# Performance work log

Hardware: AMD Instinct MI355X
Metric: run time of the kernel (lower is better)

Reference implementation:

```python
import jax, jax.numpy as jnp
import numpy as np

NUM_HEADS = 16
KEY_DIM = 64
D_MODEL = 1024
SUPPORTS = 128


def _gaussian_orthogonal_random_matrix(m, d, seed=0):
    # GOR sampler with scaling=0: orthogonal blocks, rows rescaled by norms of iid Gaussian rows.
    rng = np.random.RandomState(seed)
    blocks = []
    n_full = m // d
    for _ in range(n_full):
        q, _ = np.linalg.qr(rng.randn(d, d))
        blocks.append(q.T)
    rem = m - n_full * d
    if rem > 0:
        q, _ = np.linalg.qr(rng.randn(d, d))
        blocks.append(q.T[:rem])
    W = np.concatenate(blocks, axis=0)  # [m, d], orthonormal rows per block
    multiplier = np.linalg.norm(rng.randn(m, d), axis=1)  # chi(d) row norms
    return (multiplier[:, None] * W).astype(np.float32)


def setup_inputs() -> dict:
    key0 = jax.random.key(0)
    ks = jax.random.split(key0, 12)
    B, S, D, H, K = 4, 4096, D_MODEL, NUM_HEADS, KEY_DIM
    glorot_in = lambda k, shape, fan_in, fan_out: jax.random.uniform(
        k, shape, jnp.float32, -1.0, 1.0) * np.sqrt(6.0 / (fan_in + fan_out))
    return {
        "query": jax.random.normal(ks[0], (B, S, D), jnp.float32),
        "value": jax.random.normal(ks[1], (B, S, D), jnp.float32),
        "key": jax.random.normal(ks[2], (B, S, D), jnp.float32),
        "Wq": glorot_in(ks[3], (D, H, K), D, H * K),
        "bq": jnp.zeros((H, K), jnp.float32),
        "Wk": glorot_in(ks[4], (D, H, K), D, H * K),
        "bk": jnp.zeros((H, K), jnp.float32),
        "Wv": glorot_in(ks[5], (D, H, K), D, H * K),
        "bv": jnp.zeros((H, K), jnp.float32),
        "Wo": glorot_in(ks[6], (H, K, D), H * K, D),
        "bo": jnp.zeros((D,), jnp.float32),
        "proj": jnp.asarray(_gaussian_orthogonal_random_matrix(SUPPORTS, K)),
    }


def kernel_feature_creator(data, projection, is_query):
    # FAVOR+ positive softmax-kernel features: phi(x) = exp(w.x' - |x'|^2/2 - stab)/sqrt(m)
    d = data.shape[-1]
    m = projection.shape[0]
    x = data * (d ** -0.25)  # so that q'.k' = q.k / sqrt(d)
    wx = jnp.einsum("bshk,mk->bshm", x, projection)
    diag = 0.5 * jnp.sum(x * x, axis=-1, keepdims=True)
    if is_query:
        stab = jax.lax.stop_gradient(jnp.max(wx, axis=-1, keepdims=True))
    else:
        stab = jax.lax.stop_gradient(jnp.max(wx))
    return jnp.exp(wx - diag - stab) * (m ** -0.5)


def reference(query, value, key, Wq, bq, Wk, bk, Wv, bv, Wo, bo, proj):
    # EinsumDense projections: [B,S,D] -> [B,S,H,K]
    q = jnp.einsum("bsd,dhk->bshk", query, Wq) + bq
    k = jnp.einsum("bsd,dhk->bshk", key, Wk) + bk
    v = jnp.einsum("bsd,dhk->bshk", value, Wv) + bv
    phi_q = kernel_feature_creator(q, proj, True)   # [B,T,H,M]
    phi_k = kernel_feature_creator(k, proj, False)  # [B,S,H,M]
    kv = jnp.einsum("bshm,bshd->bhmd", phi_k, v)
    qkv = jnp.einsum("bthm,bhmd->bthd", phi_q, kv)
    # normalisation: D = phi_q . (sum_s phi_k)
    k1 = jnp.sum(phi_k, axis=1)                     # [B,H,M]
    denom = jnp.einsum("bthm,bhm->bth", phi_q, k1)
    out = qkv * (1.0 / (denom + 1e-6))[..., None]
    return jnp.einsum("bthd,hdo->bto", out, Wo) + bo
```

## Files before the change

### kernel.cpp

```cpp
#include <hip/hip_runtime.h>
#include <hip/hip_bf16.h>


#define B_  4
#define S_  4096
#define H_  16

#define SCALE_X 0.3535533905932738f
#define CM      0.08838834764831845f

typedef __attribute__((ext_vector_type(8))) short bf16x8;
typedef __attribute__((ext_vector_type(4))) short s16x4;
typedef __attribute__((ext_vector_type(8))) unsigned short u16x8;
typedef __attribute__((ext_vector_type(8))) _Float16 f16x8;
typedef __attribute__((ext_vector_type(4))) _Float16 f16x4;
typedef __attribute__((ext_vector_type(4))) float f32x4;

#define OFF_A    ((size_t)0)
#define OFF_B    ((size_t)16777216)
#define OFF_X    ((size_t)33554432)
#define OFF_KV   ((size_t)37814272)
#define OFF_K1   ((size_t)38338560)
#define OFF_BM   ((size_t)38346752)
#define OFF_ST   ((size_t)38347264)
#define OFF_A16  ((size_t)38347776)

__device__ __forceinline__ unsigned short f2bf(float x) {
  union { __hip_bfloat16 b; unsigned short u; } c;
  c.b = __float2bfloat16(x);
  return c.u;
}

#define MFMAB(ACC, A, B)                                               \
  ACC = __builtin_amdgcn_mfma_f32_16x16x32_bf16(A, B, ACC, 0, 0, 0)

#define GLDS(GP, LP)                                                  \
  __builtin_amdgcn_global_load_lds(                                   \
      (const __attribute__((address_space(1))) unsigned int*)(GP),    \
      (__attribute__((address_space(3))) unsigned int*)(LP), 16, 0, 0)

__device__ __forceinline__ void load_pfrag(const float* __restrict__ proj, int m,
                                           int kb, bf16x8* ph) {
  const float* p = proj + m * 64 + kb;
  float4 a = *reinterpret_cast<const float4*>(p);
  float4 b = *reinterpret_cast<const float4*>(p + 4);
  float v[8] = {a.x, a.y, a.z, a.w, b.x, b.y, b.z, b.w};
  bf16x8 h;
#pragma unroll
  for (int j = 0; j < 8; ++j) h[j] = (short)f2bf(v[j]);
  *ph = h;
}

#define STAGE_XR(XV, WANT_DIAG)                                           \
  {                                                                       \
    f16x8 xv_ = (XV);                                                     \
    u16x8 hh_;                                                            \
    float sq_ = 0.f;                                                      \
    _Pragma("unroll") for (int j = 0; j < 8; ++j) {                       \
      float vf_ = (float)xv_[j] * SCALE_X;                                \
      sq_ += vf_ * vf_;                                                   \
      hh_[j] = f2bf(vf_);                                                 \
    }                                                                     \
    *reinterpret_cast<u16x8*>(&Xh[srow][xc]) = hh_;                       \
    if (WANT_DIAG) {                                                      \
      sq_ += __shfl_xor(sq_, 1);                                          \
      sq_ += __shfl_xor(sq_, 2);                                          \
      sq_ += __shfl_xor(sq_, 4);                                          \
      if ((tid & 7) == 0) diags[srow] = 0.5f * sq_;                       \
    }                                                                     \
  }

#define WX_COMPUTE(WX)                                                       \
  _Pragma("unroll") for (int st_ = 0; st_ < 2; ++st_)                        \
  _Pragma("unroll") for (int ks_ = 0; ks_ < 2; ++ks_) {                      \
    const int rr_ = st_ * 16 + l15;                                          \
    const int cc_ = ((ks_ * 4 + lg) ^ (l15 & 7)) << 3;                       \
    bf16x8 xh_ = *reinterpret_cast<const bf16x8*>(&Xh[rr_][cc_]);            \
    _Pragma("unroll") for (int mtl_ = 0; mtl_ < 2; ++mtl_)                   \
        MFMAB(WX[st_][mtl_], xh_, ph[mtl_][ks_]);                            \
  }

__global__ __launch_bounds__(256) void cvt_f16_kernel(
    const float* __restrict__ in, _Float16* __restrict__ out) {
  const size_t stride = (size_t)gridDim.x * 256 * 8;
  for (size_t i = ((size_t)blockIdx.x * 256 + threadIdx.x) * 8; i < 16777216UL;
       i += stride) {
    float4 a = *reinterpret_cast<const float4*>(in + i);
    float4 b = *reinterpret_cast<const float4*>(in + i + 4);
    f16x8 h;
    h[0] = (_Float16)a.x; h[1] = (_Float16)a.y;
    h[2] = (_Float16)a.z; h[3] = (_Float16)a.w;
    h[4] = (_Float16)b.x; h[5] = (_Float16)b.y;
    h[6] = (_Float16)b.z; h[7] = (_Float16)b.w;
    *reinterpret_cast<f16x8*>(out + i) = h;
  }
}

__global__ __launch_bounds__(256) void wt_f16_kernel(
    const float* __restrict__ W, _Float16* __restrict__ T) {
  __shared__ float t[32][33];
  const int tx = threadIdx.x & 31, ty = threadIdx.x >> 5;
  const int k0 = blockIdx.x * 32, n0 = blockIdx.y * 32;
#pragma unroll
  for (int i = 0; i < 4; ++i)
    t[ty + 8 * i][tx] = W[(size_t)(k0 + ty + 8 * i) * 1024 + n0 + tx];
  __syncthreads();
#pragma unroll
  for (int i = 0; i < 4; ++i)
    T[(size_t)(n0 + ty + 8 * i) * 1024 + k0 + tx] = (_Float16)t[tx][ty + 8 * i];
}

template <int F16OUT>
__global__ __launch_bounds__(512) void gemm_lds(
    const _Float16* __restrict__ A16, const _Float16* __restrict__ BT,
    const float* __restrict__ bias, void* __restrict__ Cout) {
  __shared__ _Float16 As[4][256][32];
  __shared__ _Float16 Bs[4][256][32];
  const int tid = threadIdx.x;
  const int bid = blockIdx.x;
  const int m0 = (bid & 63) << 8;
  const int n0 = (bid >> 6) << 8;
  const int wave = tid >> 6, lane = tid & 63;
  const int wm = (wave >> 2) << 7;
  const int wn = (wave & 3) << 6;
  const int l15 = lane & 15, lg = lane >> 4;

  const int rlo = tid >> 2;
  const int cg = ((tid & 3) ^ ((rlo >> 1) & 3)) << 3;
  const int wqbase = wave << 10;

  const _Float16* pa = A16 + (size_t)(m0 + rlo) * 1024 + cg;
  const _Float16* pb = BT + (size_t)(n0 + rlo) * 1024 + cg;

  f32x4 acc[8][4];
#pragma unroll
  for (int i = 0; i < 8; ++i)
#pragma unroll
    for (int j = 0; j < 4; ++j) acc[i][j] = f32x4{0.f, 0.f, 0.f, 0.f};

#define STAGE_T(nb, kt)                                                   \
  {                                                                       \
    char* la = (char*)&As[nb][0][0] + wqbase;                             \
    char* lb = (char*)&Bs[nb][0][0] + wqbase;                             \
    GLDS(pa + (kt) * 32, la);                                             \
    GLDS(pa + (kt) * 32 + 131072, la + 8192);                             \
    GLDS(pb + (kt) * 32, lb);                                             \
    GLDS(pb + (kt) * 32 + 131072, lb + 8192);                             \
  }

#define PIPE_BAR(N)                                                       \
  asm volatile("s_waitcnt vmcnt(" #N ")" ::: "memory");                   \
  __builtin_amdgcn_s_barrier();                                           \
  asm volatile("" ::: "memory");                                          \
  __builtin_amdgcn_sched_barrier(0);

#define COMPUTE(cur)                                                      \
  {                                                                       \
    f16x8 bf[4];                                                          \
    _Pragma("unroll") for (int fn = 0; fn < 4; ++fn) {                    \
      const int r = wn + fn * 16 + l15;                                   \
      bf[fn] = *reinterpret_cast<const f16x8*>(                           \
          &Bs[cur][r][(lg ^ ((r >> 1) & 3)) << 3]);                       \
    }                                                                     \
    _Pragma("unroll") for (int fm = 0; fm < 8; ++fm) {                    \
      const int r = wm + fm * 16 + l15;                                   \
      f16x8 av = *reinterpret_cast<const f16x8*>(                         \
          &As[cur][r][(lg ^ ((r >> 1) & 3)) << 3]);                       \
      _Pragma("unroll") for (int fn = 0; fn < 4; ++fn)                    \
        acc[fm][fn] = __builtin_amdgcn_mfma_f32_16x16x32_f16(             \
            av, bf[fn], acc[fm][fn], 0, 0, 0);                            \
    }                                                                     \
  }

  STAGE_T(0, 0);
  STAGE_T(1, 1);

  for (int kt = 0; kt < 30; ++kt) {
    STAGE_T((kt + 2) & 3, kt + 2);
    PIPE_BAR(8);
    COMPUTE(kt & 3);
  }
  PIPE_BAR(4);
  COMPUTE(2);
  PIPE_BAR(0);
  COMPUTE(3);

#pragma unroll
  for (int fm = 0; fm < 8; ++fm) {
    const int row = m0 + wm + fm * 16 + (lg << 2);
#pragma unroll
    for (int fn = 0; fn < 4; ++fn) {
      const int col = n0 + wn + fn * 16 + l15;
      const float bc = bias[col];
      f32x4 v = acc[fm][fn];
      if (F16OUT) {
        _Float16* C = (_Float16*)Cout;
#pragma unroll
        for (int j = 0; j < 4; ++j)
          C[(size_t)(row + j) * 1024 + col] = (_Float16)(v[j] + bc);
      } else {
        float* C = (float*)Cout;
#pragma unroll
        for (int j = 0; j < 4; ++j) C[(size_t)(row + j) * 1024 + col] = v[j] + bc;
      }
    }
  }
#undef STAGE_T
#undef PIPE_BAR
#undef COMPUTE
}

__global__ __launch_bounds__(256) void wxmax_mfma_kernel(
    const _Float16* __restrict__ kproj, const float* __restrict__ proj,
    float* __restrict__ blockmax) {
  __shared__ unsigned short Xh[32][64];
  __shared__ float diags[32];
  __shared__ float redw[4];
  const int tid = threadIdx.x, blk = blockIdx.x;
  const int lane = tid & 63, w = tid >> 6;
  const int l15 = lane & 15, lg = lane >> 4;
  (void)diags;

  bf16x8 ph[2][2];
#pragma unroll
  for (int mtl = 0; mtl < 2; ++mtl)
#pragma unroll
    for (int ks = 0; ks < 2; ++ks)
      load_pfrag(proj, (2 * w + mtl) * 16 + l15, ks * 32 + lg * 8, &ph[mtl][ks]);

  float gmax = -3.4e38f;
  const int srow = tid >> 3, q8 = (tid & 7) << 3;
  const int xc = ((q8 >> 3) ^ (srow & 7)) << 3;

  f16x8 xk = *reinterpret_cast<const f16x8*>(
      kproj + (size_t)(blk * 512 + srow) * 64 + q8);

  for (int batch = 0; batch < 16; ++batch) {
    STAGE_XR(xk, false);
    f16x8 xk2;
    if (batch < 15)
      xk2 = *reinterpret_cast<const f16x8*>(
          kproj + (size_t)(blk * 512 + (batch + 1) * 32 + srow) * 64 + q8);
    __syncthreads();
    f32x4 wx[2][2];
#pragma unroll
    for (int st = 0; st < 2; ++st)
#pragma unroll
      for (int mtl = 0; mtl < 2; ++mtl) wx[st][mtl] = f32x4{0, 0, 0, 0};
    WX_COMPUTE(wx);
#pragma unroll
    for (int st = 0; st < 2; ++st)
#pragma unroll
      for (int mtl = 0; mtl < 2; ++mtl)
#pragma unroll
        for (int r = 0; r < 4; ++r) gmax = fmaxf(gmax, wx[st][mtl][r]);
    __syncthreads();
    if (batch < 15) xk = xk2;
  }
#pragma unroll
  for (int off = 32; off; off >>= 1) gmax = fmaxf(gmax, __shfl_xor(gmax, off));
  if (lane == 0) redw[w] = gmax;
  __syncthreads();
  if (tid == 0)
    blockmax[blk] = fmaxf(fmaxf(redw[0], redw[1]), fmaxf(redw[2], redw[3]));
}

__global__ __launch_bounds__(256) void maxreduce_kernel(
    const float* __restrict__ blockmax, float* __restrict__ stab, int n) {
  __shared__ float sm[256];
  float v = -3.4e38f;
  for (int i = threadIdx.x; i < n; i += 256) v = fmaxf(v, blockmax[i]);
  sm[threadIdx.x] = v;
  __syncthreads();
  for (int s = 128; s; s >>= 1) {
    if (threadIdx.x < s)
      sm[threadIdx.x] = fmaxf(sm[threadIdx.x], sm[threadIdx.x + s]);
    __syncthreads();
  }
  if (threadIdx.x == 0) *stab = sm[0];
}

__global__ __launch_bounds__(256) void kv_mfma_kernel(
    const _Float16* __restrict__ kproj, const _Float16* __restrict__ vproj,
    const float* __restrict__ proj, const float* __restrict__ stabp,
    float* __restrict__ kvpartT, float* __restrict__ k1part) {
  __shared__ unsigned short Xh[32][64];
  __shared__ float Vs[32][66];
  __shared__ unsigned short phiTh[128][40];
  __shared__ float diags[32];
  const int tid = threadIdx.x, blk = blockIdx.x;
  const int c = blk & 15, bh = blk >> 4, b = bh >> 4, h = bh & 15;
  const int lane = tid & 63, w = tid >> 6;
  const int l15 = lane & 15, lg = lane >> 4;
  const float stab = *stabp;

  bf16x8 ph[2][2];
#pragma unroll
  for (int mtl = 0; mtl < 2; ++mtl)
#pragma unroll
    for (int ks = 0; ks < 2; ++ks)
      load_pfrag(proj, (2 * w + mtl) * 16 + l15, ks * 32 + lg * 8, &ph[mtl][ks]);

  f32x4 akv[2][4];
#pragma unroll
  for (int i = 0; i < 2; ++i)
#pragma unroll
    for (int j = 0; j < 4; ++j) akv[i][j] = f32x4{0, 0, 0, 0};
  float k1acc[2] = {0.f, 0.f};

  const int srow = tid >> 3, q8 = (tid & 7) << 3;
  const int xc = ((q8 >> 3) ^ (srow & 7)) << 3;

  size_t rb = (((size_t)(b * S_ + c * 256 + srow) * H_ + h)) << 6;
  f16x8 xk = *reinterpret_cast<const f16x8*>(kproj + rb + q8);
  f16x8 xv = *reinterpret_cast<const f16x8*>(vproj + rb + q8);

  for (int batch = 0; batch < 8; ++batch) {
    STAGE_XR(xk, true);
    {
#pragma unroll
      for (int j = 0; j < 8; ++j) Vs[srow][q8 + j] = (float)xv[j];
    }
    f16x8 xk2, xv2;
    if (batch < 7) {
      const size_t rb2 =
          (((size_t)(b * S_ + c * 256 + (batch + 1) * 32 + srow) * H_ + h)) << 6;
      xk2 = *reinterpret_cast<const f16x8*>(kproj + rb2 + q8);
      xv2 = *reinterpret_cast<const f16x8*>(vproj + rb2 + q8);
    }
    __syncthreads();

    f32x4 wx[2][2];
#pragma unroll
    for (int st = 0; st < 2; ++st)
#pragma unroll
      for (int mtl = 0; mtl < 2; ++mtl) wx[st][mtl] = f32x4{0, 0, 0, 0};
    WX_COMPUTE(wx);

#pragma unroll
    for (int st = 0; st < 2; ++st)
#pragma unroll
      for (int mtl = 0; mtl < 2; ++mtl) {
        const int m = (2 * w + mtl) * 16 + l15;
        s16x4 hv;
        float psum = 0.f;
#pragma unroll
        for (int r = 0; r < 4; ++r) {
          const int s = st * 16 + lg * 4 + r;
          float p = __expf(wx[st][mtl][r] - diags[s] - stab) * CM;
          psum += p;
          hv[r] = (short)f2bf(p);
        }
        k1acc[mtl] += psum;
        *reinterpret_cast<s16x4*>(&phiTh[m][st * 16 + lg * 4]) = hv;
      }
    __syncthreads();

    bf16x8 pah[2];
#pragma unroll
    for (int mtl = 0; mtl < 2; ++mtl)
      pah[mtl] = *reinterpret_cast<const bf16x8*>(
          &phiTh[(2 * w + mtl) * 16 + l15][lg * 8]);
#pragma unroll
    for (int dt = 0; dt < 4; ++dt) {
      bf16x8 bvh;
#pragma unroll
      for (int j = 0; j < 8; ++j)
        bvh[j] = (short)f2bf(Vs[lg * 8 + j][dt * 16 + l15]);
#pragma unroll
      for (int mtl = 0; mtl < 2; ++mtl) MFMAB(akv[mtl][dt], pah[mtl], bvh);
    }
    __syncthreads();
    if (batch < 7) {
      xk = xk2;
      xv = xv2;
    }
  }

#pragma unroll
  for (int mtl = 0; mtl < 2; ++mtl) {
#pragma unroll
    for (int dt = 0; dt < 4; ++dt) {
      const int d = dt * 16 + l15, m0 = (2 * w + mtl) * 16 + lg * 4;
      *reinterpret_cast<f32x4*>(&kvpartT[(size_t)blk * 8192 + d * 128 + m0]) =
          akv[mtl][dt];
    }
    float kk = k1acc[mtl];
    kk += __shfl_xor(kk, 16);
    kk += __shfl_xor(kk, 32);
    if (lane < 16) k1part[blk * 128 + (2 * w + mtl) * 16 + lane] = kk;
  }
}

__global__ __launch_bounds__(256) void kvreduce_kernel(
    const float* __restrict__ kvpartT, const float* __restrict__ k1part,
    unsigned short* __restrict__ kvT, float* __restrict__ k1) {
  const int bh = blockIdx.x;
  for (int i = threadIdx.x; i < 8192; i += 256) {
    float s = 0.f;
#pragma unroll
    for (int c = 0; c < 16; ++c) s += kvpartT[(size_t)(bh * 16 + c) * 8192 + i];
    kvT[(size_t)bh * 8192 + i] = f2bf(s);
  }
  if (threadIdx.x < 128) {
    float s = 0.f;
#pragma unroll
    for (int c = 0; c < 16; ++c) s += k1part[(bh * 16 + c) * 128 + threadIdx.x];
    k1[bh * 128 + threadIdx.x] = s;
  }
}

__global__ __launch_bounds__(256) void qkv_wave_kernel(
    const _Float16* __restrict__ qproj, const unsigned short* __restrict__ kvT,
    const float* __restrict__ k1g, const float* __restrict__ proj,
    _Float16* __restrict__ outh) {
  __shared__ unsigned short Pl[128][64];
  __shared__ unsigned short Kl[64][128];
  __shared__ unsigned short Phw[4][16][128];
  __shared__ float k1s[128];
  __shared__ float dgw[4][16];
  __shared__ float dnw[4][16];
  const int tid = threadIdx.x, blk = blockIdx.x;
  const int ch = blk & 31, bh = blk >> 5, b = bh >> 4, h = bh & 15;
  const int lane = tid & 63, w = tid >> 6;
  const int l15 = lane & 15, lg = lane >> 4;

  {
    const int r = tid >> 1;
    const int cb = (tid & 1) << 2;
#pragma unroll
    for (int j = 0; j < 4; ++j) {
      const int ck = cb + j;
      float4 a = *reinterpret_cast<const float4*>(proj + r * 64 + ck * 8);
      float4 bq = *reinterpret_cast<const float4*>(proj + r * 64 + ck * 8 + 4);
      float v[8] = {a.x, a.y, a.z, a.w, bq.x, bq.y, bq.z, bq.w};
      u16x8 hh;
#pragma unroll
      for (int q = 0; q < 8; ++q) hh[q] = f2bf(v[q]);
      *reinterpret_cast<u16x8*>(&Pl[r][(ck ^ (r & 7)) << 3]) = hh;
    }
    const int d = tid >> 2;
    const int kb = (tid & 3) << 2;
#pragma unroll
    for (int j = 0; j < 4; ++j) {
      const int ck = kb + j;
      u16x8 kk = *reinterpret_cast<const u16x8*>(
          kvT + (size_t)bh * 8192 + d * 128 + ck * 8);
      *reinterpret_cast<u16x8*>(&Kl[d][(ck ^ (d & 7)) << 3]) = kk;
    }
    if (tid < 128) k1s[tid] = k1g[bh * 128 + tid];
  }
  __syncthreads();

  float k1v[8];
#pragma unroll
  for (int mt = 0; mt < 8; ++mt) k1v[mt] = k1s[mt * 16 + l15];

#pragma unroll
  for (int it = 0; it < 2; ++it) {
    const int t0 = ch * 128 + w * 32 + it * 16;
    const size_t xrow = (((size_t)(b * S_ + t0 + l15) * H_ + h)) << 6;
    f16x8 x0 = *reinterpret_cast<const f16x8*>(qproj + xrow + lg * 8);
    f16x8 x1 = *reinterpret_cast<const f16x8*>(qproj + xrow + 32 + lg * 8);
    bf16x8 xb0, xb1;
    float sq = 0.f;
#pragma unroll
    for (int j = 0; j < 8; ++j) {
      float v0 = (float)x0[j] * SCALE_X;
      float v1 = (float)x1[j] * SCALE_X;
      sq += v0 * v0 + v1 * v1;
      xb0[j] = (short)f2bf(v0);
      xb1[j] = (short)f2bf(v1);
    }
    sq += __shfl_xor(sq, 16);
    sq += __shfl_xor(sq, 32);
    if (lg == 0) dgw[w][l15] = 0.5f * sq;

    f32x4 wxa[8];
#pragma unroll
    for (int mt = 0; mt < 8; ++mt) {
      wxa[mt] = f32x4{0.f, 0.f, 0.f, 0.f};
      bf16x8 p0 = *reinterpret_cast<const bf16x8*>(
          &Pl[mt * 16 + l15][((lg) ^ (l15 & 7)) << 3]);
      bf16x8 p1 = *reinterpret_cast<const bf16x8*>(
          &Pl[mt * 16 + l15][((4 + lg) ^ (l15 & 7)) << 3]);
      MFMAB(wxa[mt], xb0, p0);
      MFMAB(wxa[mt], xb1, p1);
    }

    float rmx[4];
#pragma unroll
    for (int r = 0; r < 4; ++r) {
      float v = wxa[0][r];
#pragma unroll
      for (int mt = 1; mt < 8; ++mt) v = fmaxf(v, wxa[mt][r]);
      v = fmaxf(v, __shfl_xor(v, 1));
      v = fmaxf(v, __shfl_xor(v, 2));
      v = fmaxf(v, __shfl_xor(v, 4));
      v = fmaxf(v, __shfl_xor(v, 8));
      rmx[r] = v;
    }
    float den[4] = {0.f, 0.f, 0.f, 0.f};
#pragma unroll
    for (int r = 0; r < 4; ++r) {
      const int trow = lg * 4 + r;
      const float off = rmx[r] + dgw[w][trow];
#pragma unroll
      for (int mt = 0; mt < 8; ++mt) {
        const int m = mt * 16 + l15;
        float p = __expf(wxa[mt][r] - off) * CM;
        den[r] += p * k1v[mt];
        Phw[w][trow][((((m >> 3)) ^ (trow & 7)) << 3) | (m & 7)] = f2bf(p);
      }
    }
#pragma unroll
    for (int r = 0; r < 4; ++r) {
      float v = den[r];
      v += __shfl_xor(v, 1);
      v += __shfl_xor(v, 2);
      v += __shfl_xor(v, 4);
      v += __shfl_xor(v, 8);
      if (l15 == 0) dnw[w][lg * 4 + r] = v;
    }

    const float dens = 1.f / (dnw[w][l15] + 1e-6f);
#pragma unroll
    for (int dt = 0; dt < 4; ++dt) {
      f32x4 od = {0.f, 0.f, 0.f, 0.f};
#pragma unroll
      for (int ks = 0; ks < 4; ++ks) {
        bf16x8 ka = *reinterpret_cast<const bf16x8*>(
            &Kl[dt * 16 + l15][((ks * 4 + lg) ^ (l15 & 7)) << 3]);
        bf16x8 bp = *reinterpret_cast<const bf16x8*>(
            &Phw[w][l15][((ks * 4 + lg) ^ (l15 & 7)) << 3]);
        MFMAB(od, ka, bp);
      }
      f16x4 o;
#pragma unroll
      for (int j = 0; j < 4; ++j) o[j] = (_Float16)(od[j] * dens);
      *reinterpret_cast<f16x4*>(
          &outh[(size_t)(b * S_ + t0 + l15) * 1024 + h * 64 + dt * 16 +
                lg * 4]) = o;
    }
  }
}

extern "C" void kernel_launch(void* const* d_in, const int* in_sizes, int n_in,
                              void* d_out, int out_size, void* d_ws,
                              size_t ws_size, hipStream_t stream) {
  const float* query = (const float*)d_in[0];
  const float* value = (const float*)d_in[1];
  const float* key   = (const float*)d_in[2];
  const float* Wq = (const float*)d_in[3];
  const float* bq = (const float*)d_in[4];
  const float* Wk = (const float*)d_in[5];
  const float* bk = (const float*)d_in[6];
  const float* Wv = (const float*)d_in[7];
  const float* bv = (const float*)d_in[8];
  const float* Wo = (const float*)d_in[9];
  const float* bo = (const float*)d_in[10];
  const float* proj = (const float*)d_in[11];
  float* out = (float*)d_out;
  float* ws = (float*)d_ws;

  _Float16* KP16 = (_Float16*)(ws + OFF_A);
  _Float16* VP16 = (_Float16*)(ws + OFF_B);
  _Float16* WT = (_Float16*)(ws + OFF_X);
  float* K1P = ws + OFF_X;
  unsigned short* KVT = (unsigned short*)(ws + OFF_KV);
  float* K1 = ws + OFF_K1;
  float* BMX = ws + OFF_BM;
  float* ST = ws + OFF_ST;
  _Float16* X16 = (_Float16*)(ws + OFF_A16);
  float* KVPT = ws + OFF_A16;

  dim3 gw(32, 32);

  cvt_f16_kernel<<<2048, 256, 0, stream>>>(key, X16);
  wt_f16_kernel<<<gw, 256, 0, stream>>>(Wk, WT);
  gemm_lds<1><<<256, 512, 0, stream>>>(X16, WT, bk, KP16);
  wxmax_mfma_kernel<<<512, 256, 0, stream>>>(KP16, proj, BMX);
  maxreduce_kernel<<<1, 256, 0, stream>>>(BMX, ST, 512);
  cvt_f16_kernel<<<2048, 256, 0, stream>>>(value, X16);
  wt_f16_kernel<<<gw, 256, 0, stream>>>(Wv, WT);
  gemm_lds<1><<<256, 512, 0, stream>>>(X16, WT, bv, VP16);
  kv_mfma_kernel<<<1024, 256, 0, stream>>>(KP16, VP16, proj, ST, KVPT, K1P);
  kvreduce_kernel<<<64, 256, 0, stream>>>(KVPT, K1P, KVT, K1);
  cvt_f16_kernel<<<2048, 256, 0, stream>>>(query, X16);
  wt_f16_kernel<<<gw, 256, 0, stream>>>(Wq, WT);
  gemm_lds<1><<<256, 512, 0, stream>>>(X16, WT, bq, KP16);
  qkv_wave_kernel<<<2048, 256, 0, stream>>>(KP16, KVT, K1, proj, X16);
  wt_f16_kernel<<<gw, 256, 0, stream>>>(Wo, WT);
  gemm_lds<0><<<256, 512, 0, stream>>>(X16, WT, bo, out);
}
```

Baseline: 301.7 us.

## Stage only A in LDS with K-tile 64, load B straight into registers

The projection GEMM stops staging B through shared memory. Each wave now loads its B fragments directly from global memory into double-buffered registers, one step ahead. A is staged in a 4-deep LDS ring with a wider 64-element K tile and an XOR swizzle over 8 column groups, which halves the number of pipeline barriers. The aim is to cut LDS traffic and synchronisation per K step. In exchange, B is read redundantly from global/L2 by the waves that share the same column block, more registers are used, and the A buffer needs 128KB of LDS.

New measurement: 326.8 us. 1.08x slower.

```diff
diff --git a/kernel.cpp b/kernel.cpp
--- a/kernel.cpp
+++ b/kernel.cpp
@@ -114,8 +114,7 @@
 __global__ __launch_bounds__(512) void gemm_lds(
     const _Float16* __restrict__ A16, const _Float16* __restrict__ BT,
     const float* __restrict__ bias, void* __restrict__ Cout) {
-  __shared__ _Float16 As[4][256][32];
-  __shared__ _Float16 Bs[4][256][32];
+  __shared__ _Float16 As[4][256][64];
   const int tid = threadIdx.x;
   const int bid = blockIdx.x;
   const int m0 = (bid & 63) << 8;
@@ -125,12 +124,10 @@
   const int wn = (wave & 3) << 6;
   const int l15 = lane & 15, lg = lane >> 4;
 
-  const int rlo = tid >> 2;
-  const int cg = ((tid & 3) ^ ((rlo >> 1) & 3)) << 3;
-  const int wqbase = wave << 10;
-
-  const _Float16* pa = A16 + (size_t)(m0 + rlo) * 1024 + cg;
-  const _Float16* pb = BT + (size_t)(n0 + rlo) * 1024 + cg;
+  const int rs = tid >> 3, cs = tid & 7;
+  const int csw = (cs ^ (rs & 7)) << 3;
+  const _Float16* pa = A16 + (size_t)(m0 + rs) * 1024 + csw;
+  const int wqbase = (wave << 6) * 16;
 
   f32x4 acc[8][4];
 #pragma unroll
@@ -138,14 +135,23 @@
 #pragma unroll
     for (int j = 0; j < 4; ++j) acc[i][j] = f32x4{0.f, 0.f, 0.f, 0.f};
 
-#define STAGE_T(nb, kt)                                                   \
+#define STAGEA(kt)                                                        \
   {                                                                       \
-    char* la = (char*)&As[nb][0][0] + wqbase;                             \
-    char* lb = (char*)&Bs[nb][0][0] + wqbase;                             \
-    GLDS(pa + (kt) * 32, la);                                             \
-    GLDS(pa + (kt) * 32 + 131072, la + 8192);                             \
-    GLDS(pb + (kt) * 32, lb);                                             \
-    GLDS(pb + (kt) * 32 + 131072, lb + 8192);                             \
+    char* la = (char*)&As[(kt) & 3][0][0] + wqbase;                       \
+    const _Float16* p_ = pa + (size_t)(kt) * 64;                          \
+    GLDS(p_, la);                                                         \
+    GLDS(p_ + 65536, la + 8192);                                          \
+    GLDS(p_ + 131072, la + 16384);                                        \
+    GLDS(p_ + 196608, la + 24576);                                        \
+  }
+
+#define LOADB(DST, kt)                                                    \
+  {                                                                       \
+    _Pragma("unroll") for (int ks = 0; ks < 2; ++ks)                      \
+    _Pragma("unroll") for (int fn = 0; fn < 4; ++fn)                      \
+      DST[ks][fn] = *reinterpret_cast<const f16x8*>(                      \
+          BT + (size_t)(n0 + wn + fn * 16 + l15) * 1024 + (kt) * 64 +     \
+          ks * 32 + lg * 8);                                              \
   }
 
 #define PIPE_BAR(N)                                                       \
@@ -154,36 +160,43 @@
   asm volatile("" ::: "memory");                                          \
   __builtin_amdgcn_sched_barrier(0);
 
-#define COMPUTE(cur)                                                      \
+#define COMPUTEK(cur, BB)                                                 \
   {                                                                       \
-    f16x8 bf[4];                                                          \
-    _Pragma("unroll") for (int fn = 0; fn < 4; ++fn) {                    \
-      const int r = wn + fn * 16 + l15;                                   \
-      bf[fn] = *reinterpret_cast<const f16x8*>(                           \
-          &Bs[cur][r][(lg ^ ((r >> 1) & 3)) << 3]);                       \
-    }                                                                     \
-    _Pragma("unroll") for (int fm = 0; fm < 8; ++fm) {                    \
-      const int r = wm + fm * 16 + l15;                                   \
-      f16x8 av = *reinterpret_cast<const f16x8*>(                         \
-          &As[cur][r][(lg ^ ((r >> 1) & 3)) << 3]);                       \
+    _Pragma("unroll") for (int ks = 0; ks < 2; ++ks) {                    \
+      f16x8 av[8];                                                        \
+      _Pragma("unroll") for (int fm = 0; fm < 8; ++fm) {                  \
+        const int r = wm + fm * 16 + l15;                                 \
+        av[fm] = *reinterpret_cast<const f16x8*>(                         \
+            &As[cur][r][((ks * 4 + lg) ^ (r & 7)) << 3]);                 \
+      }                                                                   \
+      _Pragma("unroll") for (int fm = 0; fm < 8; ++fm)                    \
       _Pragma("unroll") for (int fn = 0; fn < 4; ++fn)                    \
         acc[fm][fn] = __builtin_amdgcn_mfma_f32_16x16x32_f16(             \
-            av, bf[fn], acc[fm][fn], 0, 0, 0);                            \
+            av[fm], BB[ks][fn], acc[fm][fn], 0, 0, 0);                    \
     }                                                                     \
   }
 
-  STAGE_T(0, 0);
-  STAGE_T(1, 1);
-
-  for (int kt = 0; kt < 30; ++kt) {
-    STAGE_T((kt + 2) & 3, kt + 2);
-    PIPE_BAR(8);
-    COMPUTE(kt & 3);
-  }
-  PIPE_BAR(4);
-  COMPUTE(2);
+  f16x8 bA[2][4], bB[2][4];
+  STAGEA(0);
+  STAGEA(1);
+  LOADB(bA, 0);
+
+  for (int kt2 = 0; kt2 < 7; ++kt2) {
+    const int t = kt2 * 2;
+    STAGEA(t + 2);
+    LOADB(bB, t + 1);
+    PIPE_BAR(12);
+    COMPUTEK(t & 3, bA);
+    STAGEA(t + 3);
+    LOADB(bA, t + 2);
+    PIPE_BAR(12);
+    COMPUTEK((t + 1) & 3, bB);
+  }
+  LOADB(bB, 15);
+  PIPE_BAR(8);
+  COMPUTEK(2, bA);
   PIPE_BAR(0);
-  COMPUTE(3);
+  COMPUTEK(3, bB);
 
 #pragma unroll
   for (int fm = 0; fm < 8; ++fm) {
@@ -205,9 +218,10 @@
       }
     }
   }
-#undef STAGE_T
+#undef STAGEA
+#undef LOADB
 #undef PIPE_BAR
-#undef COMPUTE
+#undef COMPUTEK
 }
 
 __global__ __launch_bounds__(256) void wxmax_mfma_kernel(
```

## Split GEMM main loop into halves with interleaved staged loads and setprio

Applied to the files above, without the earlier changes.

Restructures the projection GEMM's K-loop so global-to-LDS loads for A and B of the tile two steps ahead are issued separately, interleaved between two halves of the MFMA compute with an extra barrier in the middle. MFMA sections are wrapped in s_setprio to favour compute waves. The aim is to spread memory issue across the compute and cut the stall at each per-iteration wait. It adds a second barrier per iteration and changes the vmcnt accounting, which could add sync overhead.

Result: slower. 355.1 us (+17.7%).

```diff
diff --git a/kernel.cpp b/kernel.cpp
--- a/kernel.cpp
+++ b/kernel.cpp
@@ -138,52 +138,91 @@
 #pragma unroll
     for (int j = 0; j < 4; ++j) acc[i][j] = f32x4{0.f, 0.f, 0.f, 0.f};
 
-#define STAGE_T(nb, kt)                                                   \
+#define STAGE_A(nb, kt)                                                   \
   {                                                                       \
     char* la = (char*)&As[nb][0][0] + wqbase;                             \
-    char* lb = (char*)&Bs[nb][0][0] + wqbase;                             \
     GLDS(pa + (kt) * 32, la);                                             \
     GLDS(pa + (kt) * 32 + 131072, la + 8192);                             \
+  }
+#define STAGE_B(nb, kt)                                                   \
+  {                                                                       \
+    char* lb = (char*)&Bs[nb][0][0] + wqbase;                             \
     GLDS(pb + (kt) * 32, lb);                                             \
     GLDS(pb + (kt) * 32 + 131072, lb + 8192);                             \
   }
 
-#define PIPE_BAR(N)                                                       \
+#define WAITBAR(N)                                                        \
   asm volatile("s_waitcnt vmcnt(" #N ")" ::: "memory");                   \
   __builtin_amdgcn_s_barrier();                                           \
   asm volatile("" ::: "memory");                                          \
   __builtin_amdgcn_sched_barrier(0);
 
-#define COMPUTE(cur)                                                      \
-  {                                                                       \
-    f16x8 bf[4];                                                          \
-    _Pragma("unroll") for (int fn = 0; fn < 4; ++fn) {                    \
-      const int r = wn + fn * 16 + l15;                                   \
-      bf[fn] = *reinterpret_cast<const f16x8*>(                           \
-          &Bs[cur][r][(lg ^ ((r >> 1) & 3)) << 3]);                       \
-    }                                                                     \
-    _Pragma("unroll") for (int fm = 0; fm < 8; ++fm) {                    \
-      const int r = wm + fm * 16 + l15;                                   \
-      f16x8 av = *reinterpret_cast<const f16x8*>(                         \
-          &As[cur][r][(lg ^ ((r >> 1) & 3)) << 3]);                       \
-      _Pragma("unroll") for (int fn = 0; fn < 4; ++fn)                    \
-        acc[fm][fn] = __builtin_amdgcn_mfma_f32_16x16x32_f16(             \
-            av, bf[fn], acc[fm][fn], 0, 0, 0);                            \
-    }                                                                     \
-  }
-
-  STAGE_T(0, 0);
-  STAGE_T(1, 1);
+#define BARONLY()                                                         \
+  __builtin_amdgcn_s_barrier();                                           \
+  asm volatile("" ::: "memory");                                          \
+  __builtin_amdgcn_sched_barrier(0);
+
+#define LOAD_BF(cur)                                                      \
+  _Pragma("unroll") for (int fn = 0; fn < 4; ++fn) {                      \
+    const int r = wn + fn * 16 + l15;                                     \
+    bf[fn] = *reinterpret_cast<const f16x8*>(                             \
+        &Bs[cur][r][(lg ^ ((r >> 1) & 3)) << 3]);                         \
+  }
+
+#define COMP_HALF(cur, T0)                                                \
+  _Pragma("unroll") for (int ti = (T0); ti < (T0) + 4; ++ti) {            \
+    const int r = wm + ti * 16 + l15;                                     \
+    f16x8 av = *reinterpret_cast<const f16x8*>(                           \
+        &As[cur][r][(lg ^ ((r >> 1) & 3)) << 3]);                         \
+    _Pragma("unroll") for (int fn = 0; fn < 4; ++fn)                      \
+      acc[ti][fn] = __builtin_amdgcn_mfma_f32_16x16x32_f16(               \
+          av, bf[fn], acc[ti][fn], 0, 0, 0);                              \
+  }
+
+  STAGE_A(0, 0);
+  STAGE_B(0, 0);
+  STAGE_A(1, 1);
+  STAGE_B(1, 1);
 
   for (int kt = 0; kt < 30; ++kt) {
-    STAGE_T((kt + 2) & 3, kt + 2);
-    PIPE_BAR(8);
-    COMPUTE(kt & 3);
-  }
-  PIPE_BAR(4);
-  COMPUTE(2);
-  PIPE_BAR(0);
-  COMPUTE(3);
+    const int cur = kt & 3;
+    WAITBAR(4);
+    STAGE_A((kt + 2) & 3, kt + 2);
+    f16x8 bf[4];
+    LOAD_BF(cur);
+    __builtin_amdgcn_s_setprio(1);
+    COMP_HALF(cur, 0);
+    __builtin_amdgcn_s_setprio(0);
+    BARONLY();
+    STAGE_B((kt + 2) & 3, kt + 2);
+    __builtin_amdgcn_s_setprio(1);
+    COMP_HALF(cur, 4);
+    __builtin_amdgcn_s_setprio(0);
+  }
+  {
+    WAITBAR(4);
+    f16x8 bf[4];
+    LOAD_BF(2);
+    __builtin_amdgcn_s_setprio(1);
+    COMP_HALF(2, 0);
+    __builtin_amdgcn_s_setprio(0);
+    BARONLY();
+    __builtin_amdgcn_s_setprio(1);
+    COMP_HALF(2, 4);
+    __builtin_amdgcn_s_setprio(0);
+  }
+  {
+    WAITBAR(0);
+    f16x8 bf[4];
+    LOAD_BF(3);
+    __builtin_amdgcn_s_setprio(1);
+    COMP_HALF(3, 0);
+    __builtin_amdgcn_s_setprio(0);
+    BARONLY();
+    __builtin_amdgcn_s_setprio(1);
+    COMP_HALF(3, 4);
+    __builtin_amdgcn_s_setprio(0);
+  }
 
 #pragma unroll
   for (int fm = 0; fm < 8; ++fm) {
@@ -205,9 +244,12 @@
       }
     }
   }
-#undef STAGE_T
-#undef PIPE_BAR
-#undef COMPUTE
+#undef STAGE_A
+#undef STAGE_B
+#undef WAITBAR
+#undef BARONLY
+#undef LOAD_BF
+#undef COMP_HALF
 }
 
 __global__ __launch_bounds__(256) void wxmax_mfma_kernel(
```

## Fuse global key-max into kv kernel via online rescaling

Applied to the files above, without the earlier changes.

Removes the separate pass over projected keys that computed the global max of w·k. The kv kernel now keeps a running per-wave max, rescales its partial kv and k1 accumulators whenever that max grows, and stores the local max. The reduce kernel then rescales each partial by exp(local - global) before summing. This saves one full read of K and one launch, at the cost of extra exp and multiply work per batch inside the kv loop.

New measurement: 302.8 us. About the same (+0.3%).

```diff
diff --git a/kernel.cpp b/kernel.cpp
--- a/kernel.cpp
+++ b/kernel.cpp
@@ -210,61 +210,6 @@
 #undef COMPUTE
 }
 
-__global__ __launch_bounds__(256) void wxmax_mfma_kernel(
-    const _Float16* __restrict__ kproj, const float* __restrict__ proj,
-    float* __restrict__ blockmax) {
-  __shared__ unsigned short Xh[32][64];
-  __shared__ float diags[32];
-  __shared__ float redw[4];
-  const int tid = threadIdx.x, blk = blockIdx.x;
-  const int lane = tid & 63, w = tid >> 6;
-  const int l15 = lane & 15, lg = lane >> 4;
-  (void)diags;
-
-  bf16x8 ph[2][2];
-#pragma unroll
-  for (int mtl = 0; mtl < 2; ++mtl)
-#pragma unroll
-    for (int ks = 0; ks < 2; ++ks)
-      load_pfrag(proj, (2 * w + mtl) * 16 + l15, ks * 32 + lg * 8, &ph[mtl][ks]);
-
-  float gmax = -3.4e38f;
-  const int srow = tid >> 3, q8 = (tid & 7) << 3;
-  const int xc = ((q8 >> 3) ^ (srow & 7)) << 3;
-
-  f16x8 xk = *reinterpret_cast<const f16x8*>(
-      kproj + (size_t)(blk * 512 + srow) * 64 + q8);
-
-  for (int batch = 0; batch < 16; ++batch) {
-    STAGE_XR(xk, false);
-    f16x8 xk2;
-    if (batch < 15)
-      xk2 = *reinterpret_cast<const f16x8*>(
-          kproj + (size_t)(blk * 512 + (batch + 1) * 32 + srow) * 64 + q8);
-    __syncthreads();
-    f32x4 wx[2][2];
-#pragma unroll
-    for (int st = 0; st < 2; ++st)
-#pragma unroll
-      for (int mtl = 0; mtl < 2; ++mtl) wx[st][mtl] = f32x4{0, 0, 0, 0};
-    WX_COMPUTE(wx);
-#pragma unroll
-    for (int st = 0; st < 2; ++st)
-#pragma unroll
-      for (int mtl = 0; mtl < 2; ++mtl)
-#pragma unroll
-        for (int r = 0; r < 4; ++r) gmax = fmaxf(gmax, wx[st][mtl][r]);
-    __syncthreads();
-    if (batch < 15) xk = xk2;
-  }
-#pragma unroll
-  for (int off = 32; off; off >>= 1) gmax = fmaxf(gmax, __shfl_xor(gmax, off));
-  if (lane == 0) redw[w] = gmax;
-  __syncthreads();
-  if (tid == 0)
-    blockmax[blk] = fmaxf(fmaxf(redw[0], redw[1]), fmaxf(redw[2], redw[3]));
-}
-
 __global__ __launch_bounds__(256) void maxreduce_kernel(
     const float* __restrict__ blockmax, float* __restrict__ stab, int n) {
   __shared__ float sm[256];
@@ -282,8 +227,8 @@
 
 __global__ __launch_bounds__(256) void kv_mfma_kernel(
     const _Float16* __restrict__ kproj, const _Float16* __restrict__ vproj,
-    const float* __restrict__ proj, const float* __restrict__ stabp,
-    float* __restrict__ kvpartT, float* __restrict__ k1part) {
+    const float* __restrict__ proj, float* __restrict__ kvpartT,
+    float* __restrict__ k1part, float* __restrict__ stabloc) {
   __shared__ unsigned short Xh[32][64];
   __shared__ float Vs[32][66];
   __shared__ unsigned short phiTh[128][40];
@@ -292,7 +237,6 @@
   const int c = blk & 15, bh = blk >> 4, b = bh >> 4, h = bh & 15;
   const int lane = tid & 63, w = tid >> 6;
   const int l15 = lane & 15, lg = lane >> 4;
-  const float stab = *stabp;
 
   bf16x8 ph[2][2];
 #pragma unroll
@@ -307,6 +251,7 @@
 #pragma unroll
     for (int j = 0; j < 4; ++j) akv[i][j] = f32x4{0, 0, 0, 0};
   float k1acc[2] = {0.f, 0.f};
+  float mloc = -3.4e38f;
 
   const int srow = tid >> 3, q8 = (tid & 7) << 3;
   const int xc = ((q8 >> 3) ^ (srow & 7)) << 3;
@@ -337,6 +282,28 @@
       for (int mtl = 0; mtl < 2; ++mtl) wx[st][mtl] = f32x4{0, 0, 0, 0};
     WX_COMPUTE(wx);
 
+    {
+      float bmax = -3.4e38f;
+#pragma unroll
+      for (int st = 0; st < 2; ++st)
+#pragma unroll
+        for (int mtl = 0; mtl < 2; ++mtl)
+#pragma unroll
+          for (int r = 0; r < 4; ++r) bmax = fmaxf(bmax, wx[st][mtl][r]);
+#pragma unroll
+      for (int off = 32; off; off >>= 1)
+        bmax = fmaxf(bmax, __shfl_xor(bmax, off));
+      const float mnew = fmaxf(mloc, bmax);
+      const float rs = __expf(mloc - mnew);
+#pragma unroll
+      for (int i = 0; i < 2; ++i)
+#pragma unroll
+        for (int j = 0; j < 4; ++j) akv[i][j] *= rs;
+      k1acc[0] *= rs;
+      k1acc[1] *= rs;
+      mloc = mnew;
+    }
+
 #pragma unroll
     for (int st = 0; st < 2; ++st)
 #pragma unroll
@@ -347,7 +314,7 @@
 #pragma unroll
         for (int r = 0; r < 4; ++r) {
           const int s = st * 16 + lg * 4 + r;
-          float p = __expf(wx[st][mtl][r] - diags[s] - stab) * CM;
+          float p = __expf(wx[st][mtl][r] - diags[s] - mloc) * CM;
           psum += p;
           hv[r] = (short)f2bf(p);
         }
@@ -390,22 +357,34 @@
     kk += __shfl_xor(kk, 32);
     if (lane < 16) k1part[blk * 128 + (2 * w + mtl) * 16 + lane] = kk;
   }
+  if (lane == 0) stabloc[blk * 4 + w] = mloc;
 }
 
 __global__ __launch_bounds__(256) void kvreduce_kernel(
     const float* __restrict__ kvpartT, const float* __restrict__ k1part,
+    const float* __restrict__ stabloc, const float* __restrict__ stabp,
     unsigned short* __restrict__ kvT, float* __restrict__ k1) {
+  __shared__ float fac[16][4];
   const int bh = blockIdx.x;
+  if (threadIdx.x < 64) {
+    const int c = threadIdx.x >> 2, w = threadIdx.x & 3;
+    fac[c][w] = __expf(stabloc[(bh * 16 + c) * 4 + w] - *stabp);
+  }
+  __syncthreads();
   for (int i = threadIdx.x; i < 8192; i += 256) {
+    const int wv = (i & 127) >> 5;
     float s = 0.f;
 #pragma unroll
-    for (int c = 0; c < 16; ++c) s += kvpartT[(size_t)(bh * 16 + c) * 8192 + i];
+    for (int c = 0; c < 16; ++c)
+      s += kvpartT[(size_t)(bh * 16 + c) * 8192 + i] * fac[c][wv];
     kvT[(size_t)bh * 8192 + i] = f2bf(s);
   }
   if (threadIdx.x < 128) {
+    const int wv = threadIdx.x >> 5;
     float s = 0.f;
 #pragma unroll
-    for (int c = 0; c < 16; ++c) s += k1part[(bh * 16 + c) * 128 + threadIdx.x];
+    for (int c = 0; c < 16; ++c)
+      s += k1part[(bh * 16 + c) * 128 + threadIdx.x] * fac[c][wv];
     k1[bh * 128 + threadIdx.x] = s;
   }
 }
@@ -567,9 +546,9 @@
   _Float16* VP16 = (_Float16*)(ws + OFF_B);
   _Float16* WT = (_Float16*)(ws + OFF_X);
   float* K1P = ws + OFF_X;
+  float* SL  = ws + OFF_X + 131072;
   unsigned short* KVT = (unsigned short*)(ws + OFF_KV);
   float* K1 = ws + OFF_K1;
-  float* BMX = ws + OFF_BM;
   float* ST = ws + OFF_ST;
   _Float16* X16 = (_Float16*)(ws + OFF_A16);
   float* KVPT = ws + OFF_A16;
@@ -579,13 +558,12 @@
   cvt_f16_kernel<<<2048, 256, 0, stream>>>(key, X16);
   wt_f16_kernel<<<gw, 256, 0, stream>>>(Wk, WT);
   gemm_lds<1><<<256, 512, 0, stream>>>(X16, WT, bk, KP16);
-  wxmax_mfma_kernel<<<512, 256, 0, stream>>>(KP16, proj, BMX);
-  maxreduce_kernel<<<1, 256, 0, stream>>>(BMX, ST, 512);
   cvt_f16_kernel<<<2048, 256, 0, stream>>>(value, X16);
   wt_f16_kernel<<<gw, 256, 0, stream>>>(Wv, WT);
   gemm_lds<1><<<256, 512, 0, stream>>>(X16, WT, bv, VP16);
-  kv_mfma_kernel<<<1024, 256, 0, stream>>>(KP16, VP16, proj, ST, KVPT, K1P);
-  kvreduce_kernel<<<64, 256, 0, stream>>>(KVPT, K1P, KVT, K1);
+  kv_mfma_kernel<<<1024, 256, 0, stream>>>(KP16, VP16, proj, KVPT, K1P, SL);
+  maxreduce_kernel<<<1, 256, 0, stream>>>(SL, ST, 4096);
+  kvreduce_kernel<<<64, 256, 0, stream>>>(KVPT, K1P, SL, ST, KVT, K1);
   cvt_f16_kernel<<<2048, 256, 0, stream>>>(query, X16);
   wt_f16_kernel<<<gw, 256, 0, stream>>>(Wq, WT);
   gemm_lds<1><<<256, 512, 0, stream>>>(X16, WT, bq, KP16);
```
